# Kernel tuning notes

Measured on AMD Instinct MI355X. Metric: run time of the kernel, lower is better.

The kernel has to match this reference:

```python
import jax, jax.numpy as jnp
import numpy as np

BN_EPS = 1e-5


def setup_inputs() -> dict:
    key = jax.random.key(0)
    k1, k2, k3, k4 = jax.random.split(key, 4)
    N_IN, N_OUT, K, M, C_IN, C_OUT = 500000, 125000, 27, 60000, 64, 64
    x = jax.random.normal(k1, (N_IN, C_IN), dtype=jnp.float32)
    # Per-offset conv weights, fan-in scaled like Minkowski's kaiming init
    W = jax.random.normal(k2, (K, C_IN, C_OUT), dtype=jnp.float32) * (1.0 / np.sqrt(K * C_IN))
    gamma = jnp.ones((C_OUT,), dtype=jnp.float32)
    beta = jnp.zeros((C_OUT,), dtype=jnp.float32)
    # Kernel map: for each of the 27 offsets, M (input_idx, output_idx) pairs
    in_idx = jax.random.randint(k3, (K, M), 0, N_IN, dtype=jnp.int64)
    out_idx = jax.random.randint(k4, (K, M), 0, N_OUT, dtype=jnp.int64)
    return {"x": x, "W": W, "gamma": gamma, "beta": beta,
            "in_idx": in_idx, "out_idx": out_idx, "n_out": 125000}


def reference(x, W, gamma, beta, in_idx, out_idx, n_out):
    # Sparse 3D conv via kernel map: gather -> per-offset GEMM -> scatter-add.
    C_out = W.shape[-1]
    gathered = x[in_idx]                                   # [K, M, C_in]
    contrib = jnp.einsum('kmc,kcd->kmd', gathered, W)      # [K, M, C_out]
    out = jnp.zeros((n_out, C_out), dtype=x.dtype)
    out = out.at[out_idx.reshape(-1)].add(contrib.reshape(-1, C_out))  # [N_out, C_out]
    # MinkowskiBatchNorm (training mode): per-channel batch stats over all points
    mean = jnp.mean(out, axis=0)
    var = jnp.mean(jnp.square(out - mean), axis=0)         # biased variance
    y = (out - mean) * jax.lax.rsqrt(var + BN_EPS) * gamma + beta
    return y
```

## Files before the change

### kernel.cpp

```cpp
#include <hip/hip_runtime.h>
#include <hip/hip_fp16.h>

typedef __attribute__((ext_vector_type(8))) short short8;
typedef __attribute__((ext_vector_type(4))) float f32x4;

#define K_OFF    27
#define M_PAIRS  60000
#define C_DIM    64
#define N_IN     500000
#define N_OUT_C  125000
#define BN_EPS   1e-5f
#define E_TOT    (K_OFF * M_PAIRS)

#define TILES_PER_K  ((M_PAIRS + 63) / 64)
#define TOTAL_WT     (K_OFF * TILES_PER_K)

__device__ __forceinline__ unsigned short f32_to_bf16(float f) {
    unsigned u = __float_as_uint(f);
    u += 0x7FFFu + ((u >> 16) & 1u);
    return (unsigned short)(u >> 16);
}
__device__ __forceinline__ float bf16f(unsigned short u) {
    return __uint_as_float((unsigned)u << 16);
}

#define CONTRIB_OFF 0
#define CONTRIB_BYTES ((size_t)E_TOT * C_DIM * 2)
#define WT2_OFF   (CONTRIB_OFF + CONTRIB_BYTES)
#define WT2_BYTES ((size_t)K_OFF * C_DIM * C_DIM * 2)
#define CNT_OFF   (WT2_OFF + WT2_BYTES)
#define CNT_BYTES ((size_t)N_OUT_C * 4)
#define OFF_OFF   (CNT_OFF + CNT_BYTES)
#define CUR_OFF   (OFF_OFF + CNT_BYTES)
#define BSUM_OFF  (CUR_OFF + CNT_BYTES)
#define ST2_OFF   (BSUM_OFF + 4096)
#define WS_NEED2  (ST2_OFF + 512)

#define SCAN_BS 256
#define SCAN_NB ((N_OUT_C + SCAN_BS - 1) / SCAN_BS)

__global__ __launch_bounds__(256) void conv_w2(const float* __restrict__ W,
                                               unsigned short* __restrict__ wt) {
    const int tid = blockIdx.x * blockDim.x + threadIdx.x;
    if (tid >= K_OFF * C_DIM * C_DIM) return;
    const int c = tid & 63;
    const int d = (tid >> 6) & 63;
    const int k = tid >> 12;
    wt[tid] = f32_to_bf16(W[(k << 12) + (c << 6) + d]);
}

__global__ __launch_bounds__(256) void hist_k(const int* __restrict__ out_idx,
                                              unsigned* __restrict__ cnt) {
    for (int e = blockIdx.x * blockDim.x + threadIdx.x; e < E_TOT;
         e += gridDim.x * blockDim.x)
        atomicAdd(&cnt[out_idx[e]], 1u);
}

__global__ __launch_bounds__(SCAN_BS) void scan_a(const unsigned* __restrict__ cnt,
                                                  unsigned* __restrict__ off,
                                                  unsigned* __restrict__ bsum) {
    __shared__ unsigned s[SCAN_BS];
    const int idx = blockIdx.x * SCAN_BS + threadIdx.x;
    const unsigned v = (idx < N_OUT_C) ? cnt[idx] : 0u;
    s[threadIdx.x] = v;
    __syncthreads();
    for (int d = 1; d < SCAN_BS; d <<= 1) {
        unsigned t = (threadIdx.x >= d) ? s[threadIdx.x - d] : 0u;
        __syncthreads();
        s[threadIdx.x] += t;
        __syncthreads();
    }
    if (idx < N_OUT_C) off[idx] = s[threadIdx.x] - v;
    if (threadIdx.x == SCAN_BS - 1) bsum[blockIdx.x] = s[threadIdx.x];
}

__global__ __launch_bounds__(512) void scan_b(unsigned* __restrict__ bsum) {
    __shared__ unsigned s[512];
    const unsigned v = (threadIdx.x < SCAN_NB) ? bsum[threadIdx.x] : 0u;
    s[threadIdx.x] = v;
    __syncthreads();
    for (int d = 1; d < 512; d <<= 1) {
        unsigned t = (threadIdx.x >= d) ? s[threadIdx.x - d] : 0u;
        __syncthreads();
        s[threadIdx.x] += t;
        __syncthreads();
    }
    if (threadIdx.x < SCAN_NB) bsum[threadIdx.x] = s[threadIdx.x] - v;
}

__global__ __launch_bounds__(SCAN_BS) void scan_c(unsigned* __restrict__ off,
                                                  unsigned* __restrict__ cur,
                                                  const unsigned* __restrict__ bsum) {
    const int idx = blockIdx.x * SCAN_BS + threadIdx.x;
    if (idx < N_OUT_C) {
        const unsigned o = off[idx] + bsum[blockIdx.x];
        off[idx] = o;
        cur[idx] = o;
    }
}

__global__ __launch_bounds__(256, 3) void mfma_contrib(
    const float* __restrict__ x, const unsigned short* __restrict__ wt,
    const int* __restrict__ in_idx, const int* __restrict__ out_idx,
    unsigned* __restrict__ cursor, unsigned short* __restrict__ contrib)
{
    const int gwave = blockIdx.x * 4 + (threadIdx.x >> 6);
    if (gwave >= TOTAL_WT) return;
    const int lane = threadIdx.x & 63;
    const int lg = lane >> 4;
    const int lr = lane & 15;

    const int k  = gwave / TILES_PER_K;
    const int t  = gwave % TILES_PER_K;
    const int m0 = t * 64;
    const int kbase = k * M_PAIRS;

    short8 bfr[2][4];
    const unsigned short* wtk = wt + (size_t)k * C_DIM * C_DIM;
#pragma unroll
    for (int ks = 0; ks < 2; ++ks)
#pragma unroll
        for (int ct = 0; ct < 4; ++ct)
            bfr[ks][ct] = *(const short8*)(wtk + (ct * 16 + lr) * C_DIM + ks * 32 + lg * 8);

    int pos = -1;
    {
        const int mrow = m0 + lane;
        if (mrow < M_PAIRS) {
            const int o = out_idx[kbase + mrow];
            pos = (int)atomicAdd(&cursor[o], 1u);
        }
    }

    int aidx[4];
#pragma unroll
    for (int rt = 0; rt < 4; ++rt) {
        const int m = m0 + rt * 16 + lr;
        aidx[rt] = (m < M_PAIRS) ? in_idx[kbase + m] : -1;
    }

    f32x4 acc[4][4] = {};
#pragma unroll
    for (int ks = 0; ks < 2; ++ks) {
#pragma unroll
        for (int rt = 0; rt < 4; ++rt) {
            short8 a = {};
            if (aidx[rt] >= 0) {
                const float* xr = x + (size_t)aidx[rt] * C_DIM + ks * 32 + lg * 8;
                float4 f0 = *(const float4*)xr;
                float4 f1 = *(const float4*)(xr + 4);
                a[0] = (short)f32_to_bf16(f0.x); a[1] = (short)f32_to_bf16(f0.y);
                a[2] = (short)f32_to_bf16(f0.z); a[3] = (short)f32_to_bf16(f0.w);
                a[4] = (short)f32_to_bf16(f1.x); a[5] = (short)f32_to_bf16(f1.y);
                a[6] = (short)f32_to_bf16(f1.z); a[7] = (short)f32_to_bf16(f1.w);
            }
#pragma unroll
            for (int ct = 0; ct < 4; ++ct)
                acc[rt][ct] = __builtin_amdgcn_mfma_f32_16x16x32_bf16(
                    a, bfr[ks][ct], acc[rt][ct], 0, 0, 0);
        }
    }

#pragma unroll
    for (int rt = 0; rt < 4; ++rt) {
#pragma unroll
        for (int j = 0; j < 4; ++j) {
            const int r = rt * 16 + lg * 4 + j;
            const int p = __shfl(pos, r);
#pragma unroll
            for (int ct = 0; ct < 4; ++ct) {
                const float v0 = acc[rt][ct][j];
                const float v1 = __shfl_xor(v0, 1);
                if (((lane & 1) == 0) && p >= 0) {
                    const unsigned pk = (unsigned)f32_to_bf16(v0)
                                      | ((unsigned)f32_to_bf16(v1) << 16);
                    *(unsigned*)(contrib + (size_t)p * C_DIM + ct * 16 + lr) = pk;
                }
            }
        }
    }
}

__global__ __launch_bounds__(256) void reduce_bn(
    const unsigned short* __restrict__ contrib, const unsigned* __restrict__ off,
    const unsigned* __restrict__ cnt, float* __restrict__ out,
    float* __restrict__ stats)
{
    __shared__ float ls[128];
    if (threadIdx.x < 128) ls[threadIdx.x] = 0.f;
    __syncthreads();
    const int lane = threadIdx.x & 63;
    const int wv   = threadIdx.x >> 6;
    float ssum = 0.f, ssq = 0.f;
    for (int o = blockIdx.x * 4 + wv; o < N_OUT_C; o += gridDim.x * 4) {
        const unsigned base = off[o];
        const unsigned n    = cnt[o];
        const unsigned short* p = contrib + (size_t)base * C_DIM + lane;
        float a0 = 0.f, a1 = 0.f;
        unsigned i = 0;
        for (; i + 2 <= n; i += 2) {
            a0 += bf16f(p[(size_t)i * C_DIM]);
            a1 += bf16f(p[(size_t)(i + 1) * C_DIM]);
        }
        if (i < n) a0 += bf16f(p[(size_t)i * C_DIM]);
        const float acc = a0 + a1;
        out[(size_t)o * C_DIM + lane] = acc;
        ssum += acc;
        ssq = fmaf(acc, acc, ssq);
    }
    atomicAdd(&ls[lane], ssum);
    atomicAdd(&ls[64 + lane], ssq);
    __syncthreads();
    if (threadIdx.x < 128) unsafeAtomicAdd(&stats[threadIdx.x], ls[threadIdx.x]);
}

__global__ __launch_bounds__(256) void bn_apply_f32(
    float* __restrict__ out, const float* __restrict__ stats,
    const float* __restrict__ gamma, const float* __restrict__ beta)
{
    __shared__ float ssc[C_DIM], ssh[C_DIM];
    if (threadIdx.x < C_DIM) {
        const float inv_n = 1.0f / (float)N_OUT_C;
        float mean = stats[threadIdx.x] * inv_n;
        float var  = stats[C_DIM + threadIdx.x] * inv_n - mean * mean;
        float inv  = rsqrtf(var + BN_EPS);
        float s    = inv * gamma[threadIdx.x];
        ssc[threadIdx.x] = s;
        ssh[threadIdx.x] = beta[threadIdx.x] - mean * s;
    }
    __syncthreads();
    const int tid = blockIdx.x * blockDim.x + threadIdx.x;
    const int T   = gridDim.x * blockDim.x;
    const int cq  = (tid & 15) * 4;
    const int total4 = N_OUT_C * C_DIM / 4;
    const float4 sc = make_float4(ssc[cq], ssc[cq+1], ssc[cq+2], ssc[cq+3]);
    const float4 sh = make_float4(ssh[cq], ssh[cq+1], ssh[cq+2], ssh[cq+3]);
    float4* o4 = (float4*)out;
    for (int i = tid; i < total4; i += T) {
        float4 v = o4[i];
        v.x = fmaf(v.x, sc.x, sh.x);
        v.y = fmaf(v.y, sc.y, sh.y);
        v.z = fmaf(v.z, sc.z, sh.z);
        v.w = fmaf(v.w, sc.w, sh.w);
        o4[i] = v;
    }
}

#define XB_BYTES ((size_t)N_IN * C_DIM * 2)
#define WT_OFF   XB_BYTES
#define WT_BYTES ((size_t)K_OFF * C_DIM * C_DIM * 2)
#define AC_OFF   (WT_OFF + WT_BYTES)
#define AC_BYTES ((size_t)N_OUT_C * C_DIM * 2)
#define ST_OFF   (AC_OFF + AC_BYTES)
#define WS_NEED  (ST_OFF + 512)

__global__ __launch_bounds__(256) void conv_x(const float* __restrict__ x,
                                              unsigned short* __restrict__ xb) {
    const int tid = blockIdx.x * blockDim.x + threadIdx.x;
    const int T   = gridDim.x * blockDim.x;
    const int n4  = N_IN * C_DIM / 4;
    const float4* x4 = (const float4*)x;
    ushort4* b4 = (ushort4*)xb;
    for (int i = tid; i < n4; i += T) {
        float4 v = x4[i];
        ushort4 o;
        o.x = f32_to_bf16(v.x); o.y = f32_to_bf16(v.y);
        o.z = f32_to_bf16(v.z); o.w = f32_to_bf16(v.w);
        b4[i] = o;
    }
}

__global__ __launch_bounds__(256, 3) void mfma_scatter(
    const unsigned short* __restrict__ xb, const unsigned short* __restrict__ wt,
    const int* __restrict__ in_idx, const int* __restrict__ out_idx,
    __half2* __restrict__ acc16)
{
    const int gwave = blockIdx.x * 4 + (threadIdx.x >> 6);
    if (gwave >= TOTAL_WT) return;
    const int lane = threadIdx.x & 63;
    const int lg = lane >> 4;
    const int lr = lane & 15;
    const int k  = gwave / TILES_PER_K;
    const int t  = gwave % TILES_PER_K;
    const int m0 = t * 64;
    const int kbase = k * M_PAIRS;

    short8 bfr[2][4];
    const unsigned short* wtk = wt + (size_t)k * C_DIM * C_DIM;
#pragma unroll
    for (int ks = 0; ks < 2; ++ks)
#pragma unroll
        for (int ct = 0; ct < 4; ++ct)
            bfr[ks][ct] = *(const short8*)(wtk + (ct * 16 + lr) * C_DIM + ks * 32 + lg * 8);

    int aidx[4];
#pragma unroll
    for (int rt = 0; rt < 4; ++rt) {
        const int m = m0 + rt * 16 + lr;
        aidx[rt] = (m < M_PAIRS) ? in_idx[kbase + m] : -1;
    }

    f32x4 acc[4][4] = {};
#pragma unroll
    for (int ks = 0; ks < 2; ++ks) {
#pragma unroll
        for (int rt = 0; rt < 4; ++rt) {
            short8 a = {};
            if (aidx[rt] >= 0)
                a = *(const short8*)(xb + (size_t)aidx[rt] * C_DIM + ks * 32 + lg * 8);
#pragma unroll
            for (int ct = 0; ct < 4; ++ct)
                acc[rt][ct] = __builtin_amdgcn_mfma_f32_16x16x32_bf16(
                    a, bfr[ks][ct], acc[rt][ct], 0, 0, 0);
        }
    }

#pragma unroll
    for (int rt = 0; rt < 4; ++rt) {
#pragma unroll
        for (int j = 0; j < 4; ++j) {
            const int m = m0 + rt * 16 + lg * 4 + j;
            int o = -1;
            if (m < M_PAIRS) o = out_idx[kbase + m];
#pragma unroll
            for (int ct = 0; ct < 4; ++ct) {
                float v0 = acc[rt][ct][j];
                float v1 = __shfl_xor(v0, 1);
                if (((lane & 1) == 0) && o >= 0) {
                    __half2 h = __floats2half2_rn(v0, v1);
                    unsafeAtomicAdd(acc16 + (size_t)o * 32 + (ct * 16 + lr) / 2, h);
                }
            }
        }
    }
}

__global__ __launch_bounds__(256) void bn_stats_h2(
    const __half2* __restrict__ acc, float* __restrict__ stats)
{
    const int tid = blockIdx.x * blockDim.x + threadIdx.x;
    const int T   = gridDim.x * blockDim.x;
    const int q   = tid & 15;
    float s0=0,s1=0,s2=0,s3=0,p0=0,p1=0,p2=0,p3=0;
    for (int r = tid >> 4; r < N_OUT_C; r += (T >> 4)) {
        const __half2* p = acc + (size_t)r * 32 + 2 * q;
        float2 u = __half22float2(p[0]);
        float2 v = __half22float2(p[1]);
        s0 += u.x; p0 = fmaf(u.x, u.x, p0);
        s1 += u.y; p1 = fmaf(u.y, u.y, p1);
        s2 += v.x; p2 = fmaf(v.x, v.x, p2);
        s3 += v.y; p3 = fmaf(v.y, v.y, p3);
    }
    __shared__ float ls[128];
    if (threadIdx.x < 128) ls[threadIdx.x] = 0.f;
    __syncthreads();
    const int cq = q * 4;
    atomicAdd(&ls[cq + 0], s0); atomicAdd(&ls[cq + 1], s1);
    atomicAdd(&ls[cq + 2], s2); atomicAdd(&ls[cq + 3], s3);
    atomicAdd(&ls[64 + cq + 0], p0); atomicAdd(&ls[64 + cq + 1], p1);
    atomicAdd(&ls[64 + cq + 2], p2); atomicAdd(&ls[64 + cq + 3], p3);
    __syncthreads();
    if (threadIdx.x < 128) unsafeAtomicAdd(&stats[threadIdx.x], ls[threadIdx.x]);
}

__global__ __launch_bounds__(256) void bn_apply_h2(
    const __half2* __restrict__ acc, float* __restrict__ out,
    const float* __restrict__ stats, const float* __restrict__ gamma,
    const float* __restrict__ beta)
{
    __shared__ float ssc[C_DIM], ssh[C_DIM];
    if (threadIdx.x < C_DIM) {
        const float inv_n = 1.0f / (float)N_OUT_C;
        float mean = stats[threadIdx.x] * inv_n;
        float var  = stats[C_DIM + threadIdx.x] * inv_n - mean * mean;
        float inv  = rsqrtf(var + BN_EPS);
        float s    = inv * gamma[threadIdx.x];
        ssc[threadIdx.x] = s;
        ssh[threadIdx.x] = beta[threadIdx.x] - mean * s;
    }
    __syncthreads();
    const int tid = blockIdx.x * blockDim.x + threadIdx.x;
    const int T   = gridDim.x * blockDim.x;
    const int q   = tid & 15;
    const float4 sc = make_float4(ssc[4*q], ssc[4*q+1], ssc[4*q+2], ssc[4*q+3]);
    const float4 sh = make_float4(ssh[4*q], ssh[4*q+1], ssh[4*q+2], ssh[4*q+3]);
    for (int r = tid >> 4; r < N_OUT_C; r += (T >> 4)) {
        const __half2* p = acc + (size_t)r * 32 + 2 * q;
        float2 u = __half22float2(p[0]);
        float2 v = __half22float2(p[1]);
        float4 y;
        y.x = fmaf(u.x, sc.x, sh.x);
        y.y = fmaf(u.y, sc.y, sh.y);
        y.z = fmaf(v.x, sc.z, sh.z);
        y.w = fmaf(v.y, sc.w, sh.w);
        *(float4*)(out + (size_t)r * C_DIM + 4 * q) = y;
    }
}

#define FCHUNKS  37
#define FWPK     (FCHUNKS * 4)
#define FSPAN    ((M_PAIRS + FWPK - 1) / FWPK)

__global__ __launch_bounds__(256, 4) void conv_scatter(
    const float* __restrict__ x, const float* __restrict__ W,
    const int* __restrict__ in_idx, const int* __restrict__ out_idx,
    float* __restrict__ out)
{
    const int k     = blockIdx.x / FCHUNKS;
    const int chunk = blockIdx.x % FCHUNKS;
    const int wid   = chunk * 4 + (threadIdx.x >> 6);
    const int lane  = threadIdx.x & 63;
    float wcol[C_DIM];
    const float* Wk = W + (size_t)k * C_DIM * C_DIM;
#pragma unroll
    for (int c = 0; c < C_DIM; ++c) wcol[c] = Wk[c * C_DIM + lane];
    const int kbase = k * M_PAIRS;
    const int m0 = wid * FSPAN;
    const int m1 = (m0 + FSPAN < M_PAIRS) ? m0 + FSPAN : M_PAIRS;
    for (int m = m0; m < m1; ++m) {
        int ii = __builtin_amdgcn_readfirstlane(in_idx[kbase + m]);
        int oi = __builtin_amdgcn_readfirstlane(out_idx[kbase + m]);
        const float* xr = x + (size_t)ii * C_DIM;
        float a0=0.f,a1=0.f,a2=0.f,a3=0.f;
#pragma unroll
        for (int c = 0; c < C_DIM; c += 4) {
            a0 = fmaf(xr[c+0], wcol[c+0], a0);
            a1 = fmaf(xr[c+1], wcol[c+1], a1);
            a2 = fmaf(xr[c+2], wcol[c+2], a2);
            a3 = fmaf(xr[c+3], wcol[c+3], a3);
        }
        unsafeAtomicAdd(out + (size_t)oi * C_DIM + lane, (a0+a1)+(a2+a3));
    }
}

__global__ __launch_bounds__(256) void bn_stats_f32(
    const float* __restrict__ acc, float* __restrict__ stats)
{
    const int tid = blockIdx.x * blockDim.x + threadIdx.x;
    const int T   = gridDim.x * blockDim.x;
    const int cq  = (tid & 15) * 4;
    const int total4 = N_OUT_C * C_DIM / 4;
    float s0=0,s1=0,s2=0,s3=0,q0=0,q1=0,q2=0,q3=0;
    const float4* a4 = (const float4*)acc;
    for (int i = tid; i < total4; i += T) {
        float4 v = a4[i];
        s0+=v.x; q0=fmaf(v.x,v.x,q0);
        s1+=v.y; q1=fmaf(v.y,v.y,q1);
        s2+=v.z; q2=fmaf(v.z,v.z,q2);
        s3+=v.w; q3=fmaf(v.w,v.w,q3);
    }
    __shared__ float ls[128];
    if (threadIdx.x < 128) ls[threadIdx.x] = 0.f;
    __syncthreads();
    atomicAdd(&ls[cq+0],s0); atomicAdd(&ls[cq+1],s1);
    atomicAdd(&ls[cq+2],s2); atomicAdd(&ls[cq+3],s3);
    atomicAdd(&ls[64+cq+0],q0); atomicAdd(&ls[64+cq+1],q1);
    atomicAdd(&ls[64+cq+2],q2); atomicAdd(&ls[64+cq+3],q3);
    __syncthreads();
    if (threadIdx.x < 128) unsafeAtomicAdd(&stats[threadIdx.x], ls[threadIdx.x]);
}

extern "C" void kernel_launch(void* const* d_in, const int* in_sizes, int n_in,
                              void* d_out, int out_size, void* d_ws, size_t ws_size,
                              hipStream_t stream)
{
    const float* x       = (const float*)d_in[0];
    const float* W       = (const float*)d_in[1];
    const float* gamma   = (const float*)d_in[2];
    const float* beta    = (const float*)d_in[3];
    const int*   in_idx  = (const int*)d_in[4];
    const int*   out_idx = (const int*)d_in[5];
    float* out = (float*)d_out;

    if (ws_size >= WS_NEED2) {
        unsigned short* contrib = (unsigned short*)((char*)d_ws + CONTRIB_OFF);
        unsigned short* wt      = (unsigned short*)((char*)d_ws + WT2_OFF);
        unsigned* cnt           = (unsigned*)((char*)d_ws + CNT_OFF);
        unsigned* off           = (unsigned*)((char*)d_ws + OFF_OFF);
        unsigned* cur           = (unsigned*)((char*)d_ws + CUR_OFF);
        unsigned* bsum          = (unsigned*)((char*)d_ws + BSUM_OFF);
        float* stats            = (float*)((char*)d_ws + ST2_OFF);

        hipMemsetAsync(cnt, 0, CNT_BYTES, stream);
        hipMemsetAsync(stats, 0, 128 * sizeof(float), stream);
        conv_w2<<<(K_OFF * C_DIM * C_DIM + 255) / 256, 256, 0, stream>>>(W, wt);
        hist_k<<<1024, 256, 0, stream>>>(out_idx, cnt);
        scan_a<<<SCAN_NB, SCAN_BS, 0, stream>>>(cnt, off, bsum);
        scan_b<<<1, 512, 0, stream>>>(bsum);
        scan_c<<<SCAN_NB, SCAN_BS, 0, stream>>>(off, cur, bsum);
        mfma_contrib<<<(TOTAL_WT + 3) / 4, 256, 0, stream>>>(
            x, wt, in_idx, out_idx, cur, contrib);
        reduce_bn<<<1024, 256, 0, stream>>>(contrib, off, cnt, out, stats);
        bn_apply_f32<<<1024, 256, 0, stream>>>(out, stats, gamma, beta);
    } else if (ws_size >= WS_NEED) {
        unsigned short* xb  = (unsigned short*)d_ws;
        unsigned short* wt  = (unsigned short*)((char*)d_ws + WT_OFF);
        __half2* acc16      = (__half2*)((char*)d_ws + AC_OFF);
        float* stats        = (float*)((char*)d_ws + ST_OFF);

        hipMemsetAsync(acc16, 0, AC_BYTES, stream);
        hipMemsetAsync(stats, 0, 128 * sizeof(float), stream);
        conv_x<<<2048, 256, 0, stream>>>(x, xb);
        conv_w2<<<(K_OFF * C_DIM * C_DIM + 255) / 256, 256, 0, stream>>>(W, wt);
        mfma_scatter<<<(TOTAL_WT + 3) / 4, 256, 0, stream>>>(xb, wt, in_idx, out_idx, acc16);
        bn_stats_h2<<<512, 256, 0, stream>>>(acc16, stats);
        bn_apply_h2<<<1024, 256, 0, stream>>>(acc16, out, stats, gamma, beta);
    } else {
        float* stats = (float*)d_ws;
        hipMemsetAsync(out, 0, (size_t)N_OUT_C * C_DIM * sizeof(float), stream);
        hipMemsetAsync(stats, 0, 128 * sizeof(float), stream);
        conv_scatter<<<K_OFF * FCHUNKS, 256, 0, stream>>>(x, W, in_idx, out_idx, out);
        bn_stats_f32<<<512, 256, 0, stream>>>(out, stats);
        bn_apply_f32<<<1024, 256, 0, stream>>>(out, stats, gamma, beta);
    }
}
```

Measured before the change: 428.7 us.

## Pre-convert x to bf16 for gather and widen reduce unroll and grids

When the workspace is large enough, x is converted once to bf16 in a separate pass. The MFMA contrib kernel then gathers half-size rows straight into bf16 fragments, which halves the random-gather traffic. The change also raises the occupancy hint to 4 blocks, unrolls the segmented reduction by four accumulators, doubles the hist and reduce grid sizes, and removes the old half2 atomic-scatter path. In exchange, an extra full pass over x (read 128 MB, write 64 MB) is added, and the new path needs more workspace.

```diff
diff --git a/kernel.cpp b/kernel.cpp
--- a/kernel.cpp
+++ b/kernel.cpp
@@ -1,5 +1,4 @@
 #include <hip/hip_runtime.h>
-#include <hip/hip_fp16.h>
 
 typedef __attribute__((ext_vector_type(8))) short short8;
 typedef __attribute__((ext_vector_type(4))) float f32x4;
@@ -15,6 +14,23 @@
 #define TILES_PER_K  ((M_PAIRS + 63) / 64)
 #define TOTAL_WT     (K_OFF * TILES_PER_K)
 
+#define CONTRIB_BYTES ((size_t)E_TOT * C_DIM * 2)
+#define WT_OFF    CONTRIB_BYTES
+#define WT_BYTES  ((size_t)K_OFF * C_DIM * C_DIM * 2)
+#define CNT_OFF   (WT_OFF + WT_BYTES)
+#define CNT_BYTES ((size_t)N_OUT_C * 4)
+#define OFF_OFF   (CNT_OFF + CNT_BYTES)
+#define CUR_OFF   (OFF_OFF + CNT_BYTES)
+#define BSUM_OFF  (CUR_OFF + CNT_BYTES)
+#define ST_OFF    (BSUM_OFF + 4096)
+#define XB_OFF    ((ST_OFF + 512 + 255) & ~(size_t)255)
+#define XB_BYTES  ((size_t)N_IN * C_DIM * 2)
+#define WS_MID    XB_OFF
+#define WS_FULL   (XB_OFF + XB_BYTES)
+
+#define SCAN_BS 256
+#define SCAN_NB ((N_OUT_C + SCAN_BS - 1) / SCAN_BS)
+
 __device__ __forceinline__ unsigned short f32_to_bf16(float f) {
     unsigned u = __float_as_uint(f);
     u += 0x7FFFu + ((u >> 16) & 1u);
@@ -24,20 +40,21 @@
     return __uint_as_float((unsigned)u << 16);
 }
 
-#define CONTRIB_OFF 0
-#define CONTRIB_BYTES ((size_t)E_TOT * C_DIM * 2)
-#define WT2_OFF   (CONTRIB_OFF + CONTRIB_BYTES)
-#define WT2_BYTES ((size_t)K_OFF * C_DIM * C_DIM * 2)
-#define CNT_OFF   (WT2_OFF + WT2_BYTES)
-#define CNT_BYTES ((size_t)N_OUT_C * 4)
-#define OFF_OFF   (CNT_OFF + CNT_BYTES)
-#define CUR_OFF   (OFF_OFF + CNT_BYTES)
-#define BSUM_OFF  (CUR_OFF + CNT_BYTES)
-#define ST2_OFF   (BSUM_OFF + 4096)
-#define WS_NEED2  (ST2_OFF + 512)
-
-#define SCAN_BS 256
-#define SCAN_NB ((N_OUT_C + SCAN_BS - 1) / SCAN_BS)
+__global__ __launch_bounds__(256) void conv_x(const float* __restrict__ x,
+                                              unsigned short* __restrict__ xb) {
+    const int tid = blockIdx.x * blockDim.x + threadIdx.x;
+    const int T   = gridDim.x * blockDim.x;
+    const int n4  = N_IN * C_DIM / 4;
+    const float4* x4 = (const float4*)x;
+    ushort4* b4 = (ushort4*)xb;
+    for (int i = tid; i < n4; i += T) {
+        float4 v = x4[i];
+        ushort4 o;
+        o.x = f32_to_bf16(v.x); o.y = f32_to_bf16(v.y);
+        o.z = f32_to_bf16(v.z); o.w = f32_to_bf16(v.w);
+        b4[i] = o;
+    }
+}
 
 __global__ __launch_bounds__(256) void conv_w2(const float* __restrict__ W,
                                                unsigned short* __restrict__ wt) {
@@ -99,8 +116,10 @@
     }
 }
 
-__global__ __launch_bounds__(256, 3) void mfma_contrib(
-    const float* __restrict__ x, const unsigned short* __restrict__ wt,
+template<bool BF16G>
+__global__ __launch_bounds__(256, 4) void mfma_contrib(
+    const float* __restrict__ x, const unsigned short* __restrict__ xb,
+    const unsigned short* __restrict__ wt,
     const int* __restrict__ in_idx, const int* __restrict__ out_idx,
     unsigned* __restrict__ cursor, unsigned short* __restrict__ contrib)
 {
@@ -146,13 +165,17 @@
         for (int rt = 0; rt < 4; ++rt) {
             short8 a = {};
             if (aidx[rt] >= 0) {
-                const float* xr = x + (size_t)aidx[rt] * C_DIM + ks * 32 + lg * 8;
-                float4 f0 = *(const float4*)xr;
-                float4 f1 = *(const float4*)(xr + 4);
-                a[0] = (short)f32_to_bf16(f0.x); a[1] = (short)f32_to_bf16(f0.y);
-                a[2] = (short)f32_to_bf16(f0.z); a[3] = (short)f32_to_bf16(f0.w);
-                a[4] = (short)f32_to_bf16(f1.x); a[5] = (short)f32_to_bf16(f1.y);
-                a[6] = (short)f32_to_bf16(f1.z); a[7] = (short)f32_to_bf16(f1.w);
+                if constexpr (BF16G) {
+                    a = *(const short8*)(xb + (size_t)aidx[rt] * C_DIM + ks * 32 + lg * 8);
+                } else {
+                    const float* xr = x + (size_t)aidx[rt] * C_DIM + ks * 32 + lg * 8;
+                    float4 f0 = *(const float4*)xr;
+                    float4 f1 = *(const float4*)(xr + 4);
+                    a[0] = (short)f32_to_bf16(f0.x); a[1] = (short)f32_to_bf16(f0.y);
+                    a[2] = (short)f32_to_bf16(f0.z); a[3] = (short)f32_to_bf16(f0.w);
+                    a[4] = (short)f32_to_bf16(f1.x); a[5] = (short)f32_to_bf16(f1.y);
+                    a[6] = (short)f32_to_bf16(f1.z); a[7] = (short)f32_to_bf16(f1.w);
+                }
             }
 #pragma unroll
             for (int ct = 0; ct < 4; ++ct)
@@ -191,19 +214,22 @@
     __syncthreads();
     const int lane = threadIdx.x & 63;
     const int wv   = threadIdx.x >> 6;
+    const int GW   = gridDim.x * 4;
     float ssum = 0.f, ssq = 0.f;
-    for (int o = blockIdx.x * 4 + wv; o < N_OUT_C; o += gridDim.x * 4) {
+    for (int o = blockIdx.x * 4 + wv; o < N_OUT_C; o += GW) {
         const unsigned base = off[o];
         const unsigned n    = cnt[o];
         const unsigned short* p = contrib + (size_t)base * C_DIM + lane;
-        float a0 = 0.f, a1 = 0.f;
+        float a0 = 0.f, a1 = 0.f, a2 = 0.f, a3 = 0.f;
         unsigned i = 0;
-        for (; i + 2 <= n; i += 2) {
-            a0 += bf16f(p[(size_t)i * C_DIM]);
+        for (; i + 4 <= n; i += 4) {
+            a0 += bf16f(p[(size_t)(i + 0) * C_DIM]);
             a1 += bf16f(p[(size_t)(i + 1) * C_DIM]);
-        }
-        if (i < n) a0 += bf16f(p[(size_t)i * C_DIM]);
-        const float acc = a0 + a1;
+            a2 += bf16f(p[(size_t)(i + 2) * C_DIM]);
+            a3 += bf16f(p[(size_t)(i + 3) * C_DIM]);
+        }
+        for (; i < n; ++i) a0 += bf16f(p[(size_t)i * C_DIM]);
+        const float acc = (a0 + a1) + (a2 + a3);
         out[(size_t)o * C_DIM + lane] = acc;
         ssum += acc;
         ssq = fmaf(acc, acc, ssq);
@@ -246,157 +272,6 @@
     }
 }
 
-#define XB_BYTES ((size_t)N_IN * C_DIM * 2)
-#define WT_OFF   XB_BYTES
-#define WT_BYTES ((size_t)K_OFF * C_DIM * C_DIM * 2)
-#define AC_OFF   (WT_OFF + WT_BYTES)
-#define AC_BYTES ((size_t)N_OUT_C * C_DIM * 2)
-#define ST_OFF   (AC_OFF + AC_BYTES)
-#define WS_NEED  (ST_OFF + 512)
-
-__global__ __launch_bounds__(256) void conv_x(const float* __restrict__ x,
-                                              unsigned short* __restrict__ xb) {
-    const int tid = blockIdx.x * blockDim.x + threadIdx.x;
-    const int T   = gridDim.x * blockDim.x;
-    const int n4  = N_IN * C_DIM / 4;
-    const float4* x4 = (const float4*)x;
-    ushort4* b4 = (ushort4*)xb;
-    for (int i = tid; i < n4; i += T) {
-        float4 v = x4[i];
-        ushort4 o;
-        o.x = f32_to_bf16(v.x); o.y = f32_to_bf16(v.y);
-        o.z = f32_to_bf16(v.z); o.w = f32_to_bf16(v.w);
-        b4[i] = o;
-    }
-}
-
-__global__ __launch_bounds__(256, 3) void mfma_scatter(
-    const unsigned short* __restrict__ xb, const unsigned short* __restrict__ wt,
-    const int* __restrict__ in_idx, const int* __restrict__ out_idx,
-    __half2* __restrict__ acc16)
-{
-    const int gwave = blockIdx.x * 4 + (threadIdx.x >> 6);
-    if (gwave >= TOTAL_WT) return;
-    const int lane = threadIdx.x & 63;
-    const int lg = lane >> 4;
-    const int lr = lane & 15;
-    const int k  = gwave / TILES_PER_K;
-    const int t  = gwave % TILES_PER_K;
-    const int m0 = t * 64;
-    const int kbase = k * M_PAIRS;
-
-    short8 bfr[2][4];
-    const unsigned short* wtk = wt + (size_t)k * C_DIM * C_DIM;
-#pragma unroll
-    for (int ks = 0; ks < 2; ++ks)
-#pragma unroll
-        for (int ct = 0; ct < 4; ++ct)
-            bfr[ks][ct] = *(const short8*)(wtk + (ct * 16 + lr) * C_DIM + ks * 32 + lg * 8);
-
-    int aidx[4];
-#pragma unroll
-    for (int rt = 0; rt < 4; ++rt) {
-        const int m = m0 + rt * 16 + lr;
-        aidx[rt] = (m < M_PAIRS) ? in_idx[kbase + m] : -1;
-    }
-
-    f32x4 acc[4][4] = {};
-#pragma unroll
-    for (int ks = 0; ks < 2; ++ks) {
-#pragma unroll
-        for (int rt = 0; rt < 4; ++rt) {
-            short8 a = {};
-            if (aidx[rt] >= 0)
-                a = *(const short8*)(xb + (size_t)aidx[rt] * C_DIM + ks * 32 + lg * 8);
-#pragma unroll
-            for (int ct = 0; ct < 4; ++ct)
-                acc[rt][ct] = __builtin_amdgcn_mfma_f32_16x16x32_bf16(
-                    a, bfr[ks][ct], acc[rt][ct], 0, 0, 0);
-        }
-    }
-
-#pragma unroll
-    for (int rt = 0; rt < 4; ++rt) {
-#pragma unroll
-        for (int j = 0; j < 4; ++j) {
-            const int m = m0 + rt * 16 + lg * 4 + j;
-            int o = -1;
-            if (m < M_PAIRS) o = out_idx[kbase + m];
-#pragma unroll
-            for (int ct = 0; ct < 4; ++ct) {
-                float v0 = acc[rt][ct][j];
-                float v1 = __shfl_xor(v0, 1);
-                if (((lane & 1) == 0) && o >= 0) {
-                    __half2 h = __floats2half2_rn(v0, v1);
-                    unsafeAtomicAdd(acc16 + (size_t)o * 32 + (ct * 16 + lr) / 2, h);
-                }
-            }
-        }
-    }
-}
-
-__global__ __launch_bounds__(256) void bn_stats_h2(
-    const __half2* __restrict__ acc, float* __restrict__ stats)
-{
-    const int tid = blockIdx.x * blockDim.x + threadIdx.x;
-    const int T   = gridDim.x * blockDim.x;
-    const int q   = tid & 15;
-    float s0=0,s1=0,s2=0,s3=0,p0=0,p1=0,p2=0,p3=0;
-    for (int r = tid >> 4; r < N_OUT_C; r += (T >> 4)) {
-        const __half2* p = acc + (size_t)r * 32 + 2 * q;
-        float2 u = __half22float2(p[0]);
-        float2 v = __half22float2(p[1]);
-        s0 += u.x; p0 = fmaf(u.x, u.x, p0);
-        s1 += u.y; p1 = fmaf(u.y, u.y, p1);
-        s2 += v.x; p2 = fmaf(v.x, v.x, p2);
-        s3 += v.y; p3 = fmaf(v.y, v.y, p3);
-    }
-    __shared__ float ls[128];
-    if (threadIdx.x < 128) ls[threadIdx.x] = 0.f;
-    __syncthreads();
-    const int cq = q * 4;
-    atomicAdd(&ls[cq + 0], s0); atomicAdd(&ls[cq + 1], s1);
-    atomicAdd(&ls[cq + 2], s2); atomicAdd(&ls[cq + 3], s3);
-    atomicAdd(&ls[64 + cq + 0], p0); atomicAdd(&ls[64 + cq + 1], p1);
-    atomicAdd(&ls[64 + cq + 2], p2); atomicAdd(&ls[64 + cq + 3], p3);
-    __syncthreads();
-    if (threadIdx.x < 128) unsafeAtomicAdd(&stats[threadIdx.x], ls[threadIdx.x]);
-}
-
-__global__ __launch_bounds__(256) void bn_apply_h2(
-    const __half2* __restrict__ acc, float* __restrict__ out,
-    const float* __restrict__ stats, const float* __restrict__ gamma,
-    const float* __restrict__ beta)
-{
-    __shared__ float ssc[C_DIM], ssh[C_DIM];
-    if (threadIdx.x < C_DIM) {
-        const float inv_n = 1.0f / (float)N_OUT_C;
-        float mean = stats[threadIdx.x] * inv_n;
-        float var  = stats[C_DIM + threadIdx.x] * inv_n - mean * mean;
-        float inv  = rsqrtf(var + BN_EPS);
-        float s    = inv * gamma[threadIdx.x];
-        ssc[threadIdx.x] = s;
-        ssh[threadIdx.x] = beta[threadIdx.x] - mean * s;
-    }
-    __syncthreads();
-    const int tid = blockIdx.x * blockDim.x + threadIdx.x;
-    const int T   = gridDim.x * blockDim.x;
-    const int q   = tid & 15;
-    const float4 sc = make_float4(ssc[4*q], ssc[4*q+1], ssc[4*q+2], ssc[4*q+3]);
-    const float4 sh = make_float4(ssh[4*q], ssh[4*q+1], ssh[4*q+2], ssh[4*q+3]);
-    for (int r = tid >> 4; r < N_OUT_C; r += (T >> 4)) {
-        const __half2* p = acc + (size_t)r * 32 + 2 * q;
-        float2 u = __half22float2(p[0]);
-        float2 v = __half22float2(p[1]);
-        float4 y;
-        y.x = fmaf(u.x, sc.x, sh.x);
-        y.y = fmaf(u.y, sc.y, sh.y);
-        y.z = fmaf(v.x, sc.z, sh.z);
-        y.w = fmaf(v.y, sc.w, sh.w);
-        *(float4*)(out + (size_t)r * C_DIM + 4 * q) = y;
-    }
-}
-
 #define FCHUNKS  37
 #define FWPK     (FCHUNKS * 4)
 #define FSPAN    ((M_PAIRS + FWPK - 1) / FWPK)
@@ -472,39 +347,33 @@
     const int*   out_idx = (const int*)d_in[5];
     float* out = (float*)d_out;
 
-    if (ws_size >= WS_NEED2) {
-        unsigned short* contrib = (unsigned short*)((char*)d_ws + CONTRIB_OFF);
-        unsigned short* wt      = (unsigned short*)((char*)d_ws + WT2_OFF);
+    if (ws_size >= WS_MID) {
+        unsigned short* contrib = (unsigned short*)d_ws;
+        unsigned short* wt      = (unsigned short*)((char*)d_ws + WT_OFF);
         unsigned* cnt           = (unsigned*)((char*)d_ws + CNT_OFF);
         unsigned* off           = (unsigned*)((char*)d_ws + OFF_OFF);
         unsigned* cur           = (unsigned*)((char*)d_ws + CUR_OFF);
         unsigned* bsum          = (unsigned*)((char*)d_ws + BSUM_OFF);
-        float* stats            = (float*)((char*)d_ws + ST2_OFF);
+        float* stats            = (float*)((char*)d_ws + ST_OFF);
+        unsigned short* xb      = (unsigned short*)((char*)d_ws + XB_OFF);
+        const bool full         = (ws_size >= WS_FULL);
 
         hipMemsetAsync(cnt, 0, CNT_BYTES, stream);
         hipMemsetAsync(stats, 0, 128 * sizeof(float), stream);
         conv_w2<<<(K_OFF * C_DIM * C_DIM + 255) / 256, 256, 0, stream>>>(W, wt);
-        hist_k<<<1024, 256, 0, stream>>>(out_idx, cnt);
+        if (full) conv_x<<<2048, 256, 0, stream>>>(x, xb);
+        hist_k<<<2048, 256, 0, stream>>>(out_idx, cnt);
         scan_a<<<SCAN_NB, SCAN_BS, 0, stream>>>(cnt, off, bsum);
         scan_b<<<1, 512, 0, stream>>>(bsum);
         scan_c<<<SCAN_NB, SCAN_BS, 0, stream>>>(off, cur, bsum);
-        mfma_contrib<<<(TOTAL_WT + 3) / 4, 256, 0, stream>>>(
-            x, wt, in_idx, out_idx, cur, contrib);
-        reduce_bn<<<1024, 256, 0, stream>>>(contrib, off, cnt, out, stats);
+        if (full)
+            mfma_contrib<true><<<(TOTAL_WT + 3) / 4, 256, 0, stream>>>(
+                x, xb, wt, in_idx, out_idx, cur, contrib);
+        else
+            mfma_contrib<false><<<(TOTAL_WT + 3) / 4, 256, 0, stream>>>(
+                x, xb, wt, in_idx, out_idx, cur, contrib);
+        reduce_bn<<<2048, 256, 0, stream>>>(contrib, off, cnt, out, stats);
         bn_apply_f32<<<1024, 256, 0, stream>>>(out, stats, gamma, beta);
-    } else if (ws_size >= WS_NEED) {
-        unsigned short* xb  = (unsigned short*)d_ws;
-        unsigned short* wt  = (unsigned short*)((char*)d_ws + WT_OFF);
-        __half2* acc16      = (__half2*)((char*)d_ws + AC_OFF);
-        float* stats        = (float*)((char*)d_ws + ST_OFF);
-
-        hipMemsetAsync(acc16, 0, AC_BYTES, stream);
-        hipMemsetAsync(stats, 0, 128 * sizeof(float), stream);
-        conv_x<<<2048, 256, 0, stream>>>(x, xb);
-        conv_w2<<<(K_OFF * C_DIM * C_DIM + 255) / 256, 256, 0, stream>>>(W, wt);
-        mfma_scatter<<<(TOTAL_WT + 3) / 4, 256, 0, stream>>>(xb, wt, in_idx, out_idx, acc16);
-        bn_stats_h2<<<512, 256, 0, stream>>>(acc16, stats);
-        bn_apply_h2<<<1024, 256, 0, stream>>>(acc16, out, stats, gamma, beta);
     } else {
         float* stats = (float*)d_ws;
         hipMemsetAsync(out, 0, (size_t)N_OUT_C * C_DIM * sizeof(float), stream);
```

Result: faster. 394.5 us (-8.0%).
